# Optimization experiments

Measured on AMD Instinct MI355X. Metric: run time of the kernel, lower is better.

Reference implementation:

```python
import jax, jax.numpy as jnp
import numpy as np

D_MODEL = 1024
N_HEADS = 16
D_KEY = 64
EPS = 1e-5


def setup_inputs() -> dict:
    key = jax.random.key(0)
    ks = jax.random.split(key, 12)
    d, h, dk = D_MODEL, N_HEADS, D_KEY
    s = lambda fan_in: 1.0 / np.sqrt(fan_in)
    inp = {
        "X": jax.random.normal(ks[0], (2, 2048, d), dtype=jnp.float32),
        "Wqkv": jax.random.uniform(ks[1], (d, 3 * h * dk), jnp.float32, -s(d), s(d)),
        "bqkv": jax.random.uniform(ks[2], (3 * h * dk,), jnp.float32, -s(d), s(d)),
        "Wo": jax.random.uniform(ks[3], (h * dk, d), jnp.float32, -s(h * dk), s(h * dk)),
        "bo": jax.random.uniform(ks[4], (d,), jnp.float32, -s(h * dk), s(h * dk)),
        "W1": jax.random.uniform(ks[5], (d, 4 * d), jnp.float32, -s(d), s(d)),
        "b1": jax.random.uniform(ks[6], (4 * d,), jnp.float32, -s(d), s(d)),
        "W2": jax.random.uniform(ks[7], (4 * d, d), jnp.float32, -s(4 * d), s(4 * d)),
        "b2": jax.random.uniform(ks[8], (d,), jnp.float32, -s(4 * d), s(4 * d)),
        "ln1_g": jnp.ones((d,), jnp.float32),
        "ln1_b": jnp.zeros((d,), jnp.float32),
        "ln2_g": jnp.ones((d,), jnp.float32),
        "ln2_b": jnp.zeros((d,), jnp.float32),
    }
    return inp


def _layernorm(x, g, b):
    mu = jnp.mean(x, axis=-1, keepdims=True)
    var = jnp.var(x, axis=-1, keepdims=True)
    return (x - mu) * jax.lax.rsqrt(var + EPS) * g + b


def _block(X, Wqkv, bqkv, Wo, bo, W1, b1, W2, b2, ln1_g, ln1_b, ln2_g, ln2_b):
    B, T, _ = X.shape
    h, dk = N_HEADS, D_KEY
    # --- causal multi-head self-attention on LN(X) ---
    Xn = _layernorm(X, ln1_g, ln1_b)
    qkv = (Xn @ Wqkv + bqkv).reshape(B, T, 3, h, dk)
    q, k, v = (jnp.moveaxis(qkv, 2, 0)[i].transpose(0, 2, 1, 3) for i in range(3))  # each [B,h,T,dk]
    scores = jnp.einsum("bhqd,bhkd->bhqk", q, k) / np.sqrt(dk).astype(np.float32)
    causal = jnp.tril(jnp.ones((T, T), dtype=bool))
    scores = jnp.where(causal, scores, -jnp.inf)
    attn = jax.nn.softmax(scores, axis=-1)
    ctx = jnp.einsum("bhqk,bhkd->bhqd", attn, v)  # [B,h,T,dk]
    ctx = ctx.transpose(0, 2, 1, 3).reshape(B, T, h * dk)
    atten = ctx @ Wo + bo
    X = X + atten  # dropout is identity in eval mode
    # --- FFN on LN(X) ---
    Xn2 = _layernorm(X, ln2_g, ln2_b)
    ffn = jax.nn.relu(Xn2 @ W1 + b1) @ W2 + b2
    return X + ffn


def reference(X, Wqkv, bqkv, Wo, bo, W1, b1, W2, b2, ln1_g, ln1_b, ln2_g, ln2_b):
    return _block(X, Wqkv, bqkv, Wo, bo, W1, b1, W2, b2, ln1_g, ln1_b, ln2_g, ln2_b)
```

## Files before the change

### kernel.cpp

```cpp
#include <hip/hip_runtime.h>
#include <hip/hip_bf16.h>

typedef __hip_bfloat16 bf16;
typedef __attribute__((ext_vector_type(8))) short short8;
typedef __attribute__((ext_vector_type(4))) float f32x4;

constexpr int D     = 1024;
constexpr int T     = 2048;
constexpr int BATCH = 2;
constexpr int ROWS  = BATCH * T;
constexpr int NH    = 16;
constexpr int DKEY  = 64;
constexpr int QKVN  = 3 * D;
constexpr int FFNN  = 4 * D;

static __device__ __forceinline__ float b2f(bf16 x) { return __bfloat162float(x); }
static __device__ __forceinline__ bf16  f2b(float x) { return __float2bfloat16(x); }
static __device__ __forceinline__ float loadf(const bf16* p)  { return __bfloat162float(*p); }
static __device__ __forceinline__ float loadf(const float* p) { return *p; }
static __device__ __forceinline__ float fast_exp2(float x) { return __builtin_amdgcn_exp2f(x); }
static __device__ __forceinline__ unsigned short f2bu(float x) {
    return __bfloat16_as_ushort(__float2bfloat16(x));
}

static __device__ __forceinline__ void gload_lds16(const bf16* g, unsigned short* l) {
    __builtin_amdgcn_global_load_lds(
        (const __attribute__((address_space(1))) void*)g,
        (__attribute__((address_space(3))) void*)l,
        16, 0, 0);
}

__global__ __launch_bounds__(256) void transpose_cast(const float* __restrict__ in,
                                                      bf16* __restrict__ out,
                                                      int R, int C)
{
    __shared__ float tile[32][33];
    int c0 = blockIdx.x * 32, r0 = blockIdx.y * 32;
    int tx = threadIdx.x & 31, ty = threadIdx.x >> 5;
#pragma unroll
    for (int i = 0; i < 32; i += 8)
        tile[ty + i][tx] = in[(size_t)(r0 + ty + i) * C + c0 + tx];
    __syncthreads();
#pragma unroll
    for (int i = 0; i < 32; i += 8)
        out[(size_t)(c0 + ty + i) * R + r0 + tx] = f2b(tile[tx][ty + i]);
}

template <typename TIN>
__global__ __launch_bounds__(256) void ln_kernel(const TIN* __restrict__ X,
                                                 const float* __restrict__ g,
                                                 const float* __restrict__ b,
                                                 bf16* __restrict__ out)
{
    int row = blockIdx.x;
    int tid = threadIdx.x;
    const TIN* xr = X + (size_t)row * D;
    float v[4];
#pragma unroll
    for (int i = 0; i < 4; ++i) v[i] = loadf(xr + tid + i * 256);

    float s1 = v[0] + v[1] + v[2] + v[3];
    float s2 = v[0]*v[0] + v[1]*v[1] + v[2]*v[2] + v[3]*v[3];
#pragma unroll
    for (int off = 32; off; off >>= 1) {
        s1 += __shfl_xor(s1, off);
        s2 += __shfl_xor(s2, off);
    }
    __shared__ float red[8];
    int lane = tid & 63, w = tid >> 6;
    if (lane == 0) { red[w] = s1; red[4 + w] = s2; }
    __syncthreads();
    s1 = red[0] + red[1] + red[2] + red[3];
    s2 = red[4] + red[5] + red[6] + red[7];

    float mu   = s1 * (1.0f / D);
    float var  = s2 * (1.0f / D) - mu * mu;
    float rstd = rsqrtf(var + 1e-5f);

    bf16* orow = out + (size_t)row * D;
#pragma unroll
    for (int i = 0; i < 4; ++i) {
        int c = tid + i * 256;
        orow[c] = f2b((v[i] - mu) * rstd * g[c] + b[c]);
    }
}

template <int BM, int RELU, int RES, int OUTF32, int SPLITZ = 0>
__global__ __launch_bounds__(256) void mfma_gemm(
    const bf16* __restrict__ A, const bf16* __restrict__ Bt,
    const float* __restrict__ bias, const void* __restrict__ resid,
    void* __restrict__ out, float* __restrict__ part,
    int M, int N, int K, int Kstride)
{
    constexpr int MT = BM / 32;
    __shared__ __align__(16) unsigned short As[2][BM * 32];
    __shared__ __align__(16) unsigned short Bs[2][128 * 32];

    int gx = gridDim.x, gy = gridDim.y;
    int lid = (blockIdx.z * gy + blockIdx.y) * gx + blockIdx.x;
    int nwg = gx * gy * gridDim.z;
    int chunk = nwg >> 3;
    int swz = (lid & 7) * chunk + (lid >> 3);
    int bx = swz % gx;
    int by = (swz / gx) % gy;
    int bz = swz / (gx * gy);

    int tid  = threadIdx.x;
    int m0   = by * BM, n0 = bx * 128;
    int lane = tid & 63, wave = tid >> 6;
    int wm = (wave >> 1) * (MT * 16), wn = (wave & 1) * 64;
    int c15 = lane & 15, quad = lane >> 4;

    int koff = 0;
    if constexpr (SPLITZ) koff = bz * K;

    f32x4 acc[MT][4] = {};

    int srow = lane >> 2;
    int scol = (lane & 3) * 8;
    const bf16* abase = A  + (size_t)m0 * Kstride + koff;
    const bf16* bbase = Bt + (size_t)n0 * Kstride + koff;

    auto stage = [&](int buf, int kt) {
        int ko = kt * 32;
#pragma unroll
        for (int j = 0; j < 2; ++j) {
            int r = wave * 32 + j * 16;
            gload_lds16(bbase + (size_t)(r + srow) * Kstride + ko + scol,
                        &Bs[buf][r * 32]);
        }
        if constexpr (BM == 128) {
#pragma unroll
            for (int j = 0; j < 2; ++j) {
                int r = wave * 32 + j * 16;
                gload_lds16(abase + (size_t)(r + srow) * Kstride + ko + scol,
                            &As[buf][r * 32]);
            }
        } else {
            int r = wave * 16;
            gload_lds16(abase + (size_t)(r + srow) * Kstride + ko + scol,
                        &As[buf][r * 32]);
        }
    };

    int nk = K >> 5;
    stage(0, 0);
    __syncthreads();

    for (int kt = 0; kt < nk; ++kt) {
        int buf = kt & 1;
        if (kt + 1 < nk) stage(buf ^ 1, kt + 1);

        short8 af[MT], bfr[4];
#pragma unroll
        for (int t = 0; t < MT; ++t)
            af[t]  = *(const short8*)&As[buf][(wm + t * 16 + c15) * 32 + quad * 8];
#pragma unroll
        for (int t = 0; t < 4; ++t)
            bfr[t] = *(const short8*)&Bs[buf][(wn + t * 16 + c15) * 32 + quad * 8];
#pragma unroll
        for (int mt = 0; mt < MT; ++mt)
#pragma unroll
            for (int nt = 0; nt < 4; ++nt)
                acc[mt][nt] = __builtin_amdgcn_mfma_f32_16x16x32_bf16(
                    af[mt], bfr[nt], acc[mt][nt], 0, 0, 0);

        __syncthreads();
    }

#pragma unroll
    for (int mt = 0; mt < MT; ++mt) {
#pragma unroll
        for (int nt = 0; nt < 4; ++nt) {
            f32x4 v4 = acc[mt][nt];
            int gc = n0 + wn + nt * 16 + c15;
            float bb = (!SPLITZ || bz == 0) ? bias[gc] : 0.0f;
#pragma unroll
            for (int r = 0; r < 4; ++r) {
                int gr = m0 + wm + mt * 16 + quad * 4 + r;
                float v = v4[r] + bb;
                if constexpr (RELU) v = fmaxf(v, 0.0f);
                size_t idx = (size_t)gr * N + gc;
                if constexpr (SPLITZ) {
                    if (bz == 0) {
                        v += b2f(((const bf16*)resid)[idx]);
                        ((float*)out)[idx] = v;
                    } else {
                        part[idx] = v;
                    }
                } else {
                    if constexpr (RES == 1) v += b2f(((const bf16*)resid)[idx]);
                    if constexpr (RES == 2) v += ((const float*)resid)[idx];
                    if constexpr (OUTF32) ((float*)out)[idx] = v;
                    else                  ((bf16*)out)[idx] = f2b(v);
                }
            }
        }
    }
}

__global__ __launch_bounds__(256) void add_partial(float* __restrict__ out,
                                                   const float* __restrict__ part)
{
    int i = blockIdx.x * 256 + threadIdx.x;
    f32x4 a = ((const f32x4*)out)[i];
    f32x4 p = ((const f32x4*)part)[i];
    a += p;
    ((f32x4*)out)[i] = a;
}

__global__ __launch_bounds__(256) void flash_attn(const bf16* __restrict__ qkv,
                                                  bf16* __restrict__ ctx)
{
    constexpr int KROW = 72;
    constexpr float CSC = 0.18033688011112042f;
    constexpr float MSH = 12.0f;

    __shared__ __align__(16) unsigned short Qs[64 * KROW];
    __shared__ __align__(16) unsigned short Ks[64 * KROW];
    __shared__ __align__(16) unsigned short Vt[64 * KROW];
    unsigned short* Pt = Qs;

    int bx = blockIdx.x;
    int bh = bx & 31;
    int qi = 31 - (bx >> 5);
    int h  = bh & 15, b = bh >> 4;
    int q0 = qi * 64;

    int tid = threadIdx.x, lane = tid & 63, w = tid >> 6;
    int c15 = lane & 15, quad = lane >> 4;

    const bf16* base = qkv + (size_t)b * T * QKVN;

    {
        int row = tid >> 2, qtr = tid & 3;
        const bf16* src = base + (size_t)(q0 + row) * QKVN + h * 64 + qtr * 16;
        unsigned short* dst = &Qs[row * KROW + qtr * 16];
        uint4 v0 = *(const uint4*)(src);
        uint4 v1 = *(const uint4*)(src + 8);
        *(uint4*)(dst)     = v0;
        *(uint4*)(dst + 8) = v1;
    }
    __syncthreads();

    short8 qf[2];
#pragma unroll
    for (int s = 0; s < 2; ++s)
        qf[s] = *(const short8*)&Qs[(w * 16 + c15) * KROW + s * 32 + quad * 8];

    short8 ones;
#pragma unroll
    for (int i = 0; i < 8; ++i) ones[i] = (short)0x3F80;

    f32x4 Ot[4] = {};
    f32x4 lacc  = {};

    int nkt   = q0 / 64 + 1;
    int wqmin = q0 + w * 16;

    for (int kt = 0; kt < nkt; ++kt) {
        int k0 = kt * 64;
        int key = tid >> 2, seg = tid & 3;
        const bf16* ksrc = base + (size_t)(k0 + key) * QKVN + D + h * 64 + seg * 16;
        uint4 kv0 = *(const uint4*)ksrc;
        uint4 kv1 = *(const uint4*)(ksrc + 8);
        int keyp = (tid & 31) * 2, dk0 = (tid >> 5) * 8;
        const bf16* vsrc = base + (size_t)(k0 + keyp) * QKVN + 2 * D + h * 64 + dk0;
        uint4 vv0 = *(const uint4*)vsrc;
        uint4 vv1 = *(const uint4*)(vsrc + QKVN);

        __syncthreads();
        {
            unsigned short* kd = &Ks[key * KROW + seg * 16];
            *(uint4*)kd       = kv0;
            *(uint4*)(kd + 8) = kv1;
            const unsigned short* lo = (const unsigned short*)&vv0;
            const unsigned short* hi = (const unsigned short*)&vv1;
#pragma unroll
            for (int j = 0; j < 8; ++j) {
                unsigned int pk = (unsigned int)lo[j] | ((unsigned int)hi[j] << 16);
                *(unsigned int*)&Vt[(dk0 + j) * KROW + keyp] = pk;
            }
        }
        __syncthreads();

        f32x4 St[4] = {};
#pragma unroll
        for (int s = 0; s < 2; ++s)
#pragma unroll
            for (int ktm = 0; ktm < 4; ++ktm) {
                short8 kf = *(const short8*)&Ks[(ktm * 16 + c15) * KROW + s * 32 + quad * 8];
                St[ktm] = __builtin_amdgcn_mfma_f32_16x16x32_bf16(kf, qf[s], St[ktm], 0, 0, 0);
            }

        if (kt == nkt - 1) {
            int q_g = wqmin + c15;
#pragma unroll
            for (int ktm = 0; ktm < 4; ++ktm) {
                ushort4 pk;
#pragma unroll
                for (int r = 0; r < 4; ++r) {
                    float p = fast_exp2(fmaf(St[ktm][r], CSC, -MSH));
                    if (k0 + ktm * 16 + quad * 4 + r > q_g) p = 0.0f;
                    ((unsigned short*)&pk)[r] = f2bu(p);
                }
                *(ushort4*)&Pt[(w * 16 + c15) * KROW + ktm * 16 + quad * 4] = pk;
            }
        } else {
#pragma unroll
            for (int ktm = 0; ktm < 4; ++ktm) {
                ushort4 pk;
#pragma unroll
                for (int r = 0; r < 4; ++r)
                    ((unsigned short*)&pk)[r] = f2bu(fast_exp2(fmaf(St[ktm][r], CSC, -MSH)));
                *(ushort4*)&Pt[(w * 16 + c15) * KROW + ktm * 16 + quad * 4] = pk;
            }
        }

#pragma unroll
        for (int s = 0; s < 2; ++s) {
            short8 pf = *(const short8*)&Pt[(w * 16 + c15) * KROW + s * 32 + quad * 8];
            lacc = __builtin_amdgcn_mfma_f32_16x16x32_bf16(ones, pf, lacc, 0, 0, 0);
#pragma unroll
            for (int dt = 0; dt < 4; ++dt) {
                short8 vf = *(const short8*)&Vt[(dt * 16 + c15) * KROW + s * 32 + quad * 8];
                Ot[dt] = __builtin_amdgcn_mfma_f32_16x16x32_bf16(vf, pf, Ot[dt], 0, 0, 0);
            }
        }
    }

    {
        float inv = 1.0f / lacc[0];
        int grow = b * T + q0 + w * 16 + c15;
        bf16* dst = ctx + (size_t)grow * D + h * 64 + quad * 4;
#pragma unroll
        for (int dt = 0; dt < 4; ++dt) {
            ushort4 pk;
#pragma unroll
            for (int r = 0; r < 4; ++r)
                ((unsigned short*)&pk)[r] = f2bu(Ot[dt][r] * inv);
            *(ushort4*)(dst + dt * 16) = pk;
        }
    }
}

extern "C" void kernel_launch(void* const* d_in, const int* in_sizes, int n_in,
                              void* d_out, int out_size, void* d_ws, size_t ws_size,
                              hipStream_t stream)
{
    const float* X    = (const float*)d_in[0];
    const float* Wqkv = (const float*)d_in[1];
    const float* bqkv = (const float*)d_in[2];
    const float* Wo   = (const float*)d_in[3];
    const float* bo   = (const float*)d_in[4];
    const float* W1   = (const float*)d_in[5];
    const float* b1   = (const float*)d_in[6];
    const float* W2   = (const float*)d_in[7];
    const float* b2   = (const float*)d_in[8];
    const float* ln1g = (const float*)d_in[9];
    const float* ln1b = (const float*)d_in[10];
    const float* ln2g = (const float*)d_in[11];
    const float* ln2b = (const float*)d_in[12];
    float* out = (float*)d_out;

    char* ws = (char*)d_ws;
    bf16* Wqkv_t = (bf16*)(ws + 0);
    bf16* Wo_t   = (bf16*)(ws + 6291456);
    bf16* W1_t   = (bf16*)(ws + 8388608);
    bf16* W2_t   = (bf16*)(ws + 16777216);
    bf16* Xn     = (bf16*)(ws + 25165824);
    bf16* X1     = Xn;
    bf16* qkv    = (bf16*)(ws + 33554432);
    bf16* Xn2    = (bf16*)(ws + 33554432);
    bf16* ctx    = (bf16*)(ws + 58720256);
    bf16* mid    = (bf16*)(ws + 41943040);
    float* W2part = (float*)(ws + 0);

    transpose_cast<<<dim3(QKVN / 32, D / 32), 256, 0, stream>>>(Wqkv, Wqkv_t, D, QKVN);
    transpose_cast<<<dim3(D / 32, D / 32), 256, 0, stream>>>(Wo, Wo_t, D, D);
    transpose_cast<<<dim3(FFNN / 32, D / 32), 256, 0, stream>>>(W1, W1_t, D, FFNN);
    transpose_cast<<<dim3(D / 32, FFNN / 32), 256, 0, stream>>>(W2, W2_t, FFNN, D);

    ln_kernel<float><<<ROWS, 256, 0, stream>>>(X, ln1g, ln1b, Xn);
    mfma_gemm<128, 0, 0, 0><<<dim3(QKVN / 128, ROWS / 128), 256, 0, stream>>>(
        Xn, Wqkv_t, bqkv, nullptr, qkv, nullptr, ROWS, QKVN, D, D);
    flash_attn<<<1024, 256, 0, stream>>>(qkv, ctx);
    mfma_gemm<64, 0, 2, 0><<<dim3(D / 128, ROWS / 64), 256, 0, stream>>>(
        ctx, Wo_t, bo, X, X1, nullptr, ROWS, D, D, D);
    ln_kernel<bf16><<<ROWS, 256, 0, stream>>>(X1, ln2g, ln2b, Xn2);
    mfma_gemm<128, 1, 0, 0><<<dim3(FFNN / 128, ROWS / 128), 256, 0, stream>>>(
        Xn2, W1_t, b1, nullptr, mid, nullptr, ROWS, FFNN, D, D);
    mfma_gemm<64, 0, 1, 1, 1><<<dim3(D / 128, ROWS / 64, 2), 256, 0, stream>>>(
        mid, W2_t, b2, X1, out, W2part, ROWS, D, FFNN / 2, FFNN);
    add_partial<<<ROWS * D / 4 / 256, 256, 0, stream>>>(out, W2part);
}
```

Baseline: 347.0 us.

## Vectorize layernorm, tile-group GEMM swizzle, prefetch K/V and set MFMA priority

Layernorm now loads four contiguous elements per thread with vector loads and writes packed bf16 output. The GEMM block remap groups tiles within each XCD chunk into small 2D bands for better L2 reuse. Flash attention register-prefetches the next K/V tile while computing the current one, and raises wave priority around the MFMA sections. These target memory latency and cache locality, at the cost of more live registers in the attention loop.

```diff
diff --git a/kernel.cpp b/kernel.cpp
--- a/kernel.cpp
+++ b/kernel.cpp
@@ -16,11 +16,13 @@
 
 static __device__ __forceinline__ float b2f(bf16 x) { return __bfloat162float(x); }
 static __device__ __forceinline__ bf16  f2b(float x) { return __float2bfloat16(x); }
-static __device__ __forceinline__ float loadf(const bf16* p)  { return __bfloat162float(*p); }
-static __device__ __forceinline__ float loadf(const float* p) { return *p; }
 static __device__ __forceinline__ float fast_exp2(float x) { return __builtin_amdgcn_exp2f(x); }
 static __device__ __forceinline__ unsigned short f2bu(float x) {
     return __bfloat16_as_ushort(__float2bfloat16(x));
+}
+static __device__ __forceinline__ float bits2f(unsigned short u) {
+    unsigned int w = (unsigned int)u << 16;
+    return __builtin_bit_cast(float, w);
 }
 
 static __device__ __forceinline__ void gload_lds16(const bf16* g, unsigned short* l) {
@@ -54,10 +56,19 @@
 {
     int row = blockIdx.x;
     int tid = threadIdx.x;
+    int c0  = tid * 4;
     const TIN* xr = X + (size_t)row * D;
     float v[4];
-#pragma unroll
-    for (int i = 0; i < 4; ++i) v[i] = loadf(xr + tid + i * 256);
+    if constexpr (__is_same(TIN, float)) {
+        float4 ld = *(const float4*)(xr + c0);
+        v[0] = ld.x; v[1] = ld.y; v[2] = ld.z; v[3] = ld.w;
+    } else {
+        uint2 raw = *(const uint2*)(xr + c0);
+        v[0] = bits2f((unsigned short)(raw.x & 0xffff));
+        v[1] = bits2f((unsigned short)(raw.x >> 16));
+        v[2] = bits2f((unsigned short)(raw.y & 0xffff));
+        v[3] = bits2f((unsigned short)(raw.y >> 16));
+    }
 
     float s1 = v[0] + v[1] + v[2] + v[3];
     float s2 = v[0]*v[0] + v[1]*v[1] + v[2]*v[2] + v[3]*v[3];
@@ -77,15 +88,17 @@
     float var  = s2 * (1.0f / D) - mu * mu;
     float rstd = rsqrtf(var + 1e-5f);
 
-    bf16* orow = out + (size_t)row * D;
-#pragma unroll
-    for (int i = 0; i < 4; ++i) {
-        int c = tid + i * 256;
-        orow[c] = f2b((v[i] - mu) * rstd * g[c] + b[c]);
-    }
-}
-
-template <int BM, int RELU, int RES, int OUTF32, int SPLITZ = 0>
+    float4 gv = *(const float4*)(g + c0);
+    float4 bv = *(const float4*)(b + c0);
+    ushort4 pk;
+    pk.x = f2bu((v[0] - mu) * rstd * gv.x + bv.x);
+    pk.y = f2bu((v[1] - mu) * rstd * gv.y + bv.y);
+    pk.z = f2bu((v[2] - mu) * rstd * gv.z + bv.z);
+    pk.w = f2bu((v[3] - mu) * rstd * gv.w + bv.w);
+    *(ushort4*)(out + (size_t)row * D + c0) = pk;
+}
+
+template <int BM, int RELU, int RES, int OUTF32, int SPLITZ>
 __global__ __launch_bounds__(256) void mfma_gemm(
     const bf16* __restrict__ A, const bf16* __restrict__ Bt,
     const float* __restrict__ bias, const void* __restrict__ resid,
@@ -100,10 +113,20 @@
     int lid = (blockIdx.z * gy + blockIdx.y) * gx + blockIdx.x;
     int nwg = gx * gy * gridDim.z;
     int chunk = nwg >> 3;
-    int swz = (lid & 7) * chunk + (lid >> 3);
-    int bx = swz % gx;
-    int by = (swz / gx) % gy;
-    int bz = swz / (gx * gy);
+    int xcd = lid & 7, c = lid >> 3;
+    int f;
+    if ((gx & 7) == 0 && chunk % (gx * 4) == 0) {
+        int band  = c / (gx * 4);
+        int r     = c % (gx * 4);
+        int wi    = r >> 5;
+        int inner = r & 31;
+        f = xcd * chunk + band * (gx * 4) + (inner >> 3) * gx + wi * 8 + (inner & 7);
+    } else {
+        f = xcd * chunk + c;
+    }
+    int bx = f % gx;
+    int by = (f / gx) % gy;
+    int bz = f / (gx * gy);
 
     int tid  = threadIdx.x;
     int m0   = by * BM, n0 = bx * 128;
@@ -258,16 +281,21 @@
     int nkt   = q0 / 64 + 1;
     int wqmin = q0 + w * 16;
 
+    int key = tid >> 2, seg = tid & 3;
+    int keyp = (tid & 31) * 2, dk0 = (tid >> 5) * 8;
+
+    uint4 kv0, kv1, vv0, vv1;
+    {
+        const bf16* ksrc = base + (size_t)key * QKVN + D + h * 64 + seg * 16;
+        kv0 = *(const uint4*)ksrc;
+        kv1 = *(const uint4*)(ksrc + 8);
+        const bf16* vsrc = base + (size_t)keyp * QKVN + 2 * D + h * 64 + dk0;
+        vv0 = *(const uint4*)vsrc;
+        vv1 = *(const uint4*)(vsrc + QKVN);
+    }
+
     for (int kt = 0; kt < nkt; ++kt) {
         int k0 = kt * 64;
-        int key = tid >> 2, seg = tid & 3;
-        const bf16* ksrc = base + (size_t)(k0 + key) * QKVN + D + h * 64 + seg * 16;
-        uint4 kv0 = *(const uint4*)ksrc;
-        uint4 kv1 = *(const uint4*)(ksrc + 8);
-        int keyp = (tid & 31) * 2, dk0 = (tid >> 5) * 8;
-        const bf16* vsrc = base + (size_t)(k0 + keyp) * QKVN + 2 * D + h * 64 + dk0;
-        uint4 vv0 = *(const uint4*)vsrc;
-        uint4 vv1 = *(const uint4*)(vsrc + QKVN);
 
         __syncthreads();
         {
@@ -284,7 +312,18 @@
         }
         __syncthreads();
 
+        if (kt + 1 < nkt) {
+            int k1 = k0 + 64;
+            const bf16* ksrc = base + (size_t)(k1 + key) * QKVN + D + h * 64 + seg * 16;
+            kv0 = *(const uint4*)ksrc;
+            kv1 = *(const uint4*)(ksrc + 8);
+            const bf16* vsrc = base + (size_t)(k1 + keyp) * QKVN + 2 * D + h * 64 + dk0;
+            vv0 = *(const uint4*)vsrc;
+            vv1 = *(const uint4*)(vsrc + QKVN);
+        }
+
         f32x4 St[4] = {};
+        __builtin_amdgcn_s_setprio(1);
 #pragma unroll
         for (int s = 0; s < 2; ++s)
 #pragma unroll
@@ -292,6 +331,7 @@
                 short8 kf = *(const short8*)&Ks[(ktm * 16 + c15) * KROW + s * 32 + quad * 8];
                 St[ktm] = __builtin_amdgcn_mfma_f32_16x16x32_bf16(kf, qf[s], St[ktm], 0, 0, 0);
             }
+        __builtin_amdgcn_s_setprio(0);
 
         if (kt == nkt - 1) {
             int q_g = wqmin + c15;
@@ -317,6 +357,7 @@
             }
         }
 
+        __builtin_amdgcn_s_setprio(1);
 #pragma unroll
         for (int s = 0; s < 2; ++s) {
             short8 pf = *(const short8*)&Pt[(w * 16 + c15) * KROW + s * 32 + quad * 8];
@@ -327,6 +368,7 @@
                 Ot[dt] = __builtin_amdgcn_mfma_f32_16x16x32_bf16(vf, pf, Ot[dt], 0, 0, 0);
             }
         }
+        __builtin_amdgcn_s_setprio(0);
     }
 
     {
@@ -382,13 +424,13 @@
     transpose_cast<<<dim3(D / 32, FFNN / 32), 256, 0, stream>>>(W2, W2_t, FFNN, D);
 
     ln_kernel<float><<<ROWS, 256, 0, stream>>>(X, ln1g, ln1b, Xn);
-    mfma_gemm<128, 0, 0, 0><<<dim3(QKVN / 128, ROWS / 128), 256, 0, stream>>>(
+    mfma_gemm<128, 0, 0, 0, 0><<<dim3(QKVN / 128, ROWS / 128), 256, 0, stream>>>(
         Xn, Wqkv_t, bqkv, nullptr, qkv, nullptr, ROWS, QKVN, D, D);
     flash_attn<<<1024, 256, 0, stream>>>(qkv, ctx);
-    mfma_gemm<64, 0, 2, 0><<<dim3(D / 128, ROWS / 64), 256, 0, stream>>>(
+    mfma_gemm<64, 0, 2, 0, 0><<<dim3(D / 128, ROWS / 64), 256, 0, stream>>>(
         ctx, Wo_t, bo, X, X1, nullptr, ROWS, D, D, D);
     ln_kernel<bf16><<<ROWS, 256, 0, stream>>>(X1, ln2g, ln2b, Xn2);
-    mfma_gemm<128, 1, 0, 0><<<dim3(FFNN / 128, ROWS / 128), 256, 0, stream>>>(
+    mfma_gemm<128, 1, 0, 0, 0><<<dim3(FFNN / 128, ROWS / 128), 256, 0, stream>>>(
         Xn2, W1_t, b1, nullptr, mid, nullptr, ROWS, FFNN, D, D);
     mfma_gemm<64, 0, 1, 1, 1><<<dim3(D / 128, ROWS / 64, 2), 256, 0, stream>>>(
         mid, W2_t, b2, X1, out, W2part, ROWS, D, FFNN / 2, FFNN);
```

New measurement: 349.9 us. No clear change (+0.8%).
